# Performance work log

Hardware: AMD Instinct MI355X
Metric: run time of the kernel (lower is better)

## Reference

```python
import jax, jax.numpy as jnp
import numpy as np

BETA = 0.25


def setup_inputs() -> dict:
    key = jax.random.key(0)
    k1, k2 = jax.random.split(key)
    B, T, D, K = 64, 256, 512, 8192
    latents = jax.random.normal(k1, (B, T, D), dtype=jnp.float32)
    # nn.Embedding weight initialized uniform(-1/K, 1/K)
    emb = jax.random.uniform(k2, (K, D), dtype=jnp.float32, minval=-1.0 / K, maxval=1.0 / K)
    return {"latents": latents, "emb": emb}


def reference(latents, emb):
    B, T, D = latents.shape
    K = emb.shape[0]
    flat = latents.reshape(B * T, D)  # [N, D]
    # squared euclidean distances: [N, K]
    dist = (
        jnp.sum(flat ** 2, axis=1, keepdims=True)
        + jnp.sum(emb ** 2, axis=1)
        - 2.0 * flat @ emb.T
    )
    encoding_inds = jnp.argmin(dist, axis=1)  # [N]
    # one-hot @ emb == direct gather
    quantized = emb[encoding_inds].reshape(B, T, D)
    # losses (per-token mean over feature dim)
    q_sg = jax.lax.stop_gradient(quantized)
    l_sg = jax.lax.stop_gradient(latents)
    commitment_loss = jnp.mean((q_sg - latents) ** 2, axis=-1)  # [B, T]
    embedding_loss = jnp.mean((quantized - l_sg) ** 2, axis=-1)  # [B, T]
    vq_loss = embedding_loss + BETA * commitment_loss
    # straight-through estimator
    quantized_st = latents + jax.lax.stop_gradient(quantized - latents)
    return quantized_st, vq_loss, encoding_inds[None, :]  # inds as [1, N] like .t()
```

## Files before the change

### kernel.cpp

```cpp
#include <hip/hip_runtime.h>


#define D_DIM   512
#define K_CODES 8192
#define N_TOK   16384

typedef int i32x4  __attribute__((ext_vector_type(4)));
typedef int i32x16 __attribute__((ext_vector_type(16)));

__device__ __forceinline__ float np_pairwise_sq(const float* __restrict__ a) {
    float blk[4];
#pragma unroll
    for (int b = 0; b < 4; ++b) {
        const float* p = a + b * 128;
        float r[8];
#pragma unroll
        for (int j = 0; j < 8; ++j) { double d = (double)p[j]; r[j] = (float)(d * d); }
        for (int i = 8; i < 128; i += 8) {
#pragma unroll
            for (int j = 0; j < 8; ++j) { double d = (double)p[i + j]; r[j] = r[j] + (float)(d * d); }
        }
        blk[b] = ((r[0] + r[1]) + (r[2] + r[3])) + ((r[4] + r[5]) + (r[6] + r[7]));
    }
    return (blk[0] + blk[1]) + (blk[2] + blk[3]);
}

__device__ __forceinline__ unsigned q4pack(float4 v, float sc) {
    int q0 = (int)rintf(fminf(fmaxf(v.x * sc, -127.f), 127.f));
    int q1 = (int)rintf(fminf(fmaxf(v.y * sc, -127.f), 127.f));
    int q2 = (int)rintf(fminf(fmaxf(v.z * sc, -127.f), 127.f));
    int q3 = (int)rintf(fminf(fmaxf(v.w * sc, -127.f), 127.f));
    return (unsigned)(q0 & 255) | ((unsigned)(q1 & 255) << 8)
         | ((unsigned)(q2 & 255) << 16) | ((unsigned)(q3 & 255) << 24);
}

__global__ __launch_bounds__(256) void vq_prep(
    const float* __restrict__ X, const float* __restrict__ E,
    unsigned char* __restrict__ Xq, unsigned char* __restrict__ Eq,
    float* __restrict__ sx, float* __restrict__ se)
{
    const int bid = blockIdx.x;
    const int t = threadIdx.x;
    if (bid < 2048) {
        int tid = bid * 256 + t;
        int tb = tid >> 12, rem = tid & 4095;
        int line = rem >> 6, lane = rem & 63;
        int s = line >> 2, tf = line & 3;
        int token = tb * 128 + tf * 32 + (lane & 31);
        int d0 = s * 32 + (lane >> 5) * 16;
        const float4* p = (const float4*)(X + (size_t)token * D_DIM + d0);
        const float sc = 127.0f / 6.0f;
        uint4 o = make_uint4(q4pack(p[0], sc), q4pack(p[1], sc), q4pack(p[2], sc), q4pack(p[3], sc));
        *(uint4*)(Xq + (size_t)tb * 65536 + (size_t)line * 1024 + (size_t)lane * 16) = o;
    } else if (bid < 3072) {
        int tid = (bid - 2048) * 256 + t;
        int cb = tid >> 10, rem = tid & 1023;
        int s = rem >> 6, lane = rem & 63;
        int code = cb * 32 + (lane & 31);
        int d0 = s * 32 + (lane >> 5) * 16;
        const float4* p = (const float4*)(E + (size_t)code * D_DIM + d0);
        const float sc = 1040384.0f;
        uint4 o = make_uint4(q4pack(p[0], sc), q4pack(p[1], sc), q4pack(p[2], sc), q4pack(p[3], sc));
        *(uint4*)(Eq + (size_t)cb * 16384 + (size_t)s * 1024 + (size_t)lane * 16) = o;
    } else {
        int wv = (bid - 3072) * 4 + (t >> 6);
        int sub = (t >> 5) & 1, l32 = t & 31;
        int row = wv * 2 + sub;
        const float* p;
        float* dst;
        if (row < N_TOK) { p = X + (size_t)row * D_DIM; dst = sx + row; }
        else if (row < N_TOK + K_CODES) { p = E + (size_t)(row - N_TOK) * D_DIM; dst = se + (row - N_TOK); }
        else return;
        int b = l32 >> 3, rr = l32 & 7;
        const float* q = p + b * 128 + rr;
        double d0 = (double)q[0];
        float r = (float)(d0 * d0);
#pragma unroll
        for (int i = 1; i < 16; ++i) { double d = (double)q[8 * i]; r = r + (float)(d * d); }
#pragma unroll
        for (int m = 1; m <= 16; m <<= 1) r = r + __shfl_xor(r, m);
        if (l32 == 0) *dst = r;
    }
}

#define MFMA8(A, B, C) C = __builtin_amdgcn_mfma_i32_32x32x32_i8(A, B, C, 0, 0, 0)

#define UPD(T, P) { int _p = (P); \
    int _mn = _p < m0[T] ? _p : m0[T]; \
    m1[T] = _mn > m1[T] ? _mn : m1[T]; \
    m0[T] = _p > m0[T] ? _p : m0[T]; }

#define BLOAD(d0_, d1_, d2_, d3_, sidx) { int _o = ((sidx) & 15) * 4096 + laneB; \
    d0_ = *(const i32x4*)(smemB + _o); \
    d1_ = *(const i32x4*)(smemB + _o + 1024); \
    d2_ = *(const i32x4*)(smemB + _o + 2048); \
    d3_ = *(const i32x4*)(smemB + _o + 3072); }

#define STEP(Af, B0_, B1_, B2_, B3_) { \
    MFMA8(Af, B0_, a0); MFMA8(Af, B1_, a1); MFMA8(Af, B2_, a2); MFMA8(Af, B3_, a3); }

__global__ __launch_bounds__(512, 2) void vq_gemm(
    const unsigned char* __restrict__ Xq, const unsigned char* __restrict__ Eq,
    float* __restrict__ vbuf, int* __restrict__ ibuf)
{
    __shared__ unsigned int smemU[16384];
    const int tid = threadIdx.x;
    const int lane = tid & 63, w = tid >> 6;
    const int hi5 = lane >> 5, l31 = lane & 31;
    const int laneB = lane * 16;

    const int bid  = blockIdx.x;
    const int xcd  = bid & 7, slot = bid >> 3;
    const int q    = xcd >> 2;
    const int tb   = (xcd & 3) * 32 + slot;

    const unsigned char* Ap = Eq + (size_t)(q * 128 + w) * 16384;

    i32x4 QA0 = *(const i32x4*)(Ap + 0 * 1024 + laneB);
    i32x4 QA1 = *(const i32x4*)(Ap + 1 * 1024 + laneB);
    i32x4 QA2 = *(const i32x4*)(Ap + 2 * 1024 + laneB);
    i32x4 QA3 = *(const i32x4*)(Ap + 3 * 1024 + laneB);
    i32x4 QB0 = *(const i32x4*)(Ap + 4 * 1024 + laneB);
    i32x4 QB1 = *(const i32x4*)(Ap + 5 * 1024 + laneB);
    i32x4 QB2 = *(const i32x4*)(Ap + 6 * 1024 + laneB);
    i32x4 QB3 = *(const i32x4*)(Ap + 7 * 1024 + laneB);

    {
        const unsigned char* src = Xq + (size_t)tb * 65536;
#pragma unroll
        for (int c = 0; c < 8; ++c) {
            int off  = (c * 512 + tid) * 16;
            int doff = (c * 512 + w * 64) * 16;
            __builtin_amdgcn_global_load_lds((const unsigned int*)(src + off),
                                             (unsigned int*)((unsigned char*)smemU + doff), 16, 0, 0);
        }
    }
    __syncthreads();

    const unsigned char* smemB = (const unsigned char*)smemU;

    int m0[4], m1[4];
#pragma unroll
    for (int tf = 0; tf < 4; ++tf) { m0[tf] = (int)0x80000000; m1[tf] = (int)0x80000000; }

    i32x4 BA0, BA1, BA2, BA3, BB0, BB1, BB2, BB3;
    i32x4 BC0, BC1, BC2, BC3, BD0, BD1, BD2, BD3;
    BLOAD(BA0, BA1, BA2, BA3, 0);
    BLOAD(BB0, BB1, BB2, BB3, 1);

#pragma unroll 1
    for (int ck = 0; ck < 16; ++ck) {
        i32x16 a0 = {}, a1 = {}, a2 = {}, a3 = {};

#pragma unroll 1
        for (int mq = 0; mq < 2; ++mq) {
            const int s0 = 8 * mq;
            BLOAD(BC0, BC1, BC2, BC3, s0 + 2); STEP(QA0, BA0, BA1, BA2, BA3);
            BLOAD(BD0, BD1, BD2, BD3, s0 + 3); STEP(QA1, BB0, BB1, BB2, BB3);
            BLOAD(BA0, BA1, BA2, BA3, s0 + 4); STEP(QA2, BC0, BC1, BC2, BC3);
            BLOAD(BB0, BB1, BB2, BB3, s0 + 5); STEP(QA3, BD0, BD1, BD2, BD3);
            if (mq < 1) {
                QA0 = *(const i32x4*)(Ap + (size_t)(s0 + 8)  * 1024 + laneB);
                QA1 = *(const i32x4*)(Ap + (size_t)(s0 + 9)  * 1024 + laneB);
                QA2 = *(const i32x4*)(Ap + (size_t)(s0 + 10) * 1024 + laneB);
                QA3 = *(const i32x4*)(Ap + (size_t)(s0 + 11) * 1024 + laneB);
            }
            BLOAD(BC0, BC1, BC2, BC3, s0 + 6); STEP(QB0, BA0, BA1, BA2, BA3);
            BLOAD(BD0, BD1, BD2, BD3, s0 + 7); STEP(QB1, BB0, BB1, BB2, BB3);
            BLOAD(BA0, BA1, BA2, BA3, s0 + 8); STEP(QB2, BC0, BC1, BC2, BC3);
            BLOAD(BB0, BB1, BB2, BB3, s0 + 9); STEP(QB3, BD0, BD1, BD2, BD3);
            if (mq < 1) {
                QB0 = *(const i32x4*)(Ap + (size_t)(s0 + 12) * 1024 + laneB);
                QB1 = *(const i32x4*)(Ap + (size_t)(s0 + 13) * 1024 + laneB);
                QB2 = *(const i32x4*)(Ap + (size_t)(s0 + 14) * 1024 + laneB);
                QB3 = *(const i32x4*)(Ap + (size_t)(s0 + 15) * 1024 + laneB);
            }
        }

        const unsigned char* Apn = Ap + 131072;
        if (ck < 15) {
            QA0 = *(const i32x4*)(Apn + 0 * 1024 + laneB);
            QA1 = *(const i32x4*)(Apn + 1 * 1024 + laneB);
            QA2 = *(const i32x4*)(Apn + 2 * 1024 + laneB);
            QA3 = *(const i32x4*)(Apn + 3 * 1024 + laneB);
            QB0 = *(const i32x4*)(Apn + 4 * 1024 + laneB);
            QB1 = *(const i32x4*)(Apn + 5 * 1024 + laneB);
            QB2 = *(const i32x4*)(Apn + 6 * 1024 + laneB);
            QB3 = *(const i32x4*)(Apn + 7 * 1024 + laneB);
        }
        __builtin_amdgcn_sched_barrier(0);

        const int cb = q * 128 + ck * 8 + w;
        const int binv = 8191 - (cb * 32 + 4 * hi5);
#pragma unroll
        for (int g = 0; g < 16; ++g) {
            const int bp = binv - ((g & 3) + 8 * (g >> 2));
            UPD(0, ((a0[g] >> 5) << 13) + bp);
            UPD(1, ((a1[g] >> 5) << 13) + bp);
            UPD(2, ((a2[g] >> 5) << 13) + bp);
            UPD(3, ((a3[g] >> 5) << 13) + bp);
        }
        Ap = Apn;
    }

#pragma unroll
    for (int tf = 0; tf < 4; ++tf) {
        int token = tb * 128 + tf * 32 + l31;
        int slot2 = q * 32 + w * 4 + hi5 * 2;
        size_t base = (size_t)token * 64 + slot2;
        vbuf[base]     = (float)(m0[tf] >> 13);
        ibuf[base]     = 8191 - (m0[tf] & 8191);
        vbuf[base + 1] = (float)(m1[tf] >> 13);
        ibuf[base + 1] = 8191 - (m1[tf] & 8191);
    }
}

__global__ __launch_bounds__(256) void vq_refine(
    const float* __restrict__ X, const float* __restrict__ E,
    const float* __restrict__ vbuf, const int* __restrict__ ibuf,
    const float* __restrict__ sx, const float* __restrict__ se,
    float* __restrict__ out_idx, float* __restrict__ outq, float* __restrict__ outl)
{
    int t = threadIdx.x;
    int n = blockIdx.x * 4 + (t >> 6);
    int lane = t & 63;

    float v = vbuf[(size_t)n * 64 + lane];
    int   ci = ibuf[(size_t)n * 64 + lane];
    float b0 = v;
#pragma unroll
    for (int m = 1; m <= 32; m <<= 1) b0 = fmaxf(b0, __shfl_xor(b0, m));

    unsigned long long mask = __ballot(v >= b0 - 200.0f);

    const float* xr = X + (size_t)n * D_DIM;
    float4 xa = ((const float4*)xr)[lane * 2];
    float4 xb = ((const float4*)xr)[lane * 2 + 1];
    float sxn = sx[n];

    float bd = 1e30f; int bi = 2147483647;
    while (mask) {
        int b = (int)__builtin_ctzll(mask);
        mask &= mask - 1;
        int idx = __shfl(ci, b);
        const float* er = E + (size_t)idx * D_DIM;
        float4 ea = ((const float4*)er)[lane * 2];
        float4 eb = ((const float4*)er)[lane * 2 + 1];
        double p = (double)xa.x * ea.x + (double)xa.y * ea.y + (double)xa.z * ea.z + (double)xa.w * ea.w
                 + (double)xb.x * eb.x + (double)xb.y * eb.y + (double)xb.z * eb.z + (double)xb.w * eb.w;
#pragma unroll
        for (int m = 1; m <= 32; m <<= 1) p = p + __shfl_xor(p, m);
        float M = (float)p;
        float S = sxn + se[idx];
        float d = S - 2.0f * M;
        if (d < bd || (d == bd && idx < bi)) { bd = d; bi = idx; }
    }
    if (lane == 0) out_idx[n] = (float)bi;

    const float* er = E + (size_t)bi * D_DIM;
    float4 ea = ((const float4*)er)[lane * 2];
    float4 eb = ((const float4*)er)[lane * 2 + 1];
    float4 da, db;
    da.x = ea.x - xa.x; da.y = ea.y - xa.y; da.z = ea.z - xa.z; da.w = ea.w - xa.w;
    db.x = eb.x - xb.x; db.y = eb.y - xb.y; db.z = eb.z - xb.z; db.w = eb.w - xb.w;
    float4 qa, qb;
    qa.x = xa.x + da.x; qa.y = xa.y + da.y; qa.z = xa.z + da.z; qa.w = xa.w + da.w;
    qb.x = xb.x + db.x; qb.y = xb.y + db.y; qb.z = xb.z + db.z; qb.w = xb.w + db.w;
    float4* qr = (float4*)(outq + (size_t)n * D_DIM);
    qr[lane * 2] = qa;
    qr[lane * 2 + 1] = qb;
    float s = da.x * da.x + da.y * da.y + da.z * da.z + da.w * da.w
            + db.x * db.x + db.y * db.y + db.z * db.z + db.w * db.w;
#pragma unroll
    for (int m = 1; m <= 32; m <<= 1) s += __shfl_xor(s, m);
    if (lane == 0) {
        float mmean = s * (1.0f / (float)D_DIM);
        outl[n] = mmean + 0.25f * mmean;
    }
}

__global__ __launch_bounds__(512) void vq_argmin_fb(
    const float* __restrict__ X, const float* __restrict__ E, float* __restrict__ out_idx)
{
    __shared__ __align__(16) unsigned char smem[48 * 1024];
    float4* Xs = (float4*)smem;
    float4* Es = (float4*)(smem + 16 * 1024);
    float*  cv = (float*)smem;
    int*    ci = (int*)(smem + 16 * 1024);
    const int t = threadIdx.x, tc = t & 31, tr = t >> 5;
    const int tok0 = blockIdx.x * 64;
    const float4* Xg = (const float4*)X;
    const float4* Eg = (const float4*)E;
    float v0[4], v1[4]; int i0[4], i1[4];
#pragma unroll
    for (int i = 0; i < 4; ++i) { v0[i] = -1e30f; v1[i] = -1e30f; i0[i] = 0; i1[i] = 1; }
    for (int kt = 0; kt < K_CODES / 128; ++kt) {
        float acc[4][4];
#pragma unroll
        for (int i = 0; i < 4; ++i)
#pragma unroll
            for (int j = 0; j < 4; ++j) acc[i][j] = 0.f;
        for (int dc = 0; dc < 8; ++dc) {
            __syncthreads();
#pragma unroll
            for (int s = 0; s < 2; ++s) {
                int id = t + s * 512; int rr = id >> 4, m = id & 15;
                Xs[rr * 16 + ((m + (rr >> 2)) & 15)] = Xg[(size_t)(tok0 + rr) * 128 + dc * 16 + m];
            }
#pragma unroll
            for (int s = 0; s < 4; ++s) {
                int id = t + s * 512; int rr = id >> 4, m = id & 15;
                Es[rr * 16 + ((m + (rr >> 2)) & 15)] = Eg[(size_t)(kt * 128 + rr) * 128 + dc * 16 + m];
            }
            __syncthreads();
#pragma unroll
            for (int dd4 = 0; dd4 < 16; ++dd4) {
                float4 xv[4], ev[4];
#pragma unroll
                for (int i = 0; i < 4; ++i) xv[i] = Xs[(4 * tr + i) * 16 + ((dd4 + tr) & 15)];
#pragma unroll
                for (int j = 0; j < 4; ++j) ev[j] = Es[(4 * tc + j) * 16 + ((dd4 + tc) & 15)];
#pragma unroll
                for (int i = 0; i < 4; ++i)
#pragma unroll
                    for (int j = 0; j < 4; ++j)
                        acc[i][j] += xv[i].x * ev[j].x + xv[i].y * ev[j].y + xv[i].z * ev[j].z + xv[i].w * ev[j].w;
            }
        }
#pragma unroll
        for (int i = 0; i < 4; ++i)
#pragma unroll
            for (int j = 0; j < 4; ++j) {
                float v = acc[i][j]; int idx = kt * 128 + 4 * tc + j;
                if (v > v0[i])      { v1[i] = v0[i]; i1[i] = i0[i]; v0[i] = v; i0[i] = idx; }
                else if (v > v1[i]) { v1[i] = v; i1[i] = idx; }
            }
    }
    __syncthreads();
#pragma unroll
    for (int i = 0; i < 4; ++i) {
        int row = 4 * tr + i;
        cv[row * 64 + 2 * tc] = v0[i];     ci[row * 64 + 2 * tc] = i0[i];
        cv[row * 64 + 2 * tc + 1] = v1[i]; ci[row * 64 + 2 * tc + 1] = i1[i];
    }
    __syncthreads();
    if (t < 64) {
        const int row = t;
        float b0 = -1e30f;
        for (int s = 0; s < 64; ++s) b0 = fmaxf(b0, cv[row * 64 + s]);
        const float* xr = X + (size_t)(tok0 + row) * D_DIM;
        const float sumx2 = np_pairwise_sq(xr);
        float bd = 1e30f; int bi = 0x7fffffff;
        for (int s = 0; s < 64; ++s) {
            float v = cv[row * 64 + s];
            if (v < b0 - 1.0e-4f) continue;
            int idx = ci[row * 64 + s];
            const float* er = E + (size_t)idx * D_DIM;
            double acc = 0.0;
            for (int d0 = 0; d0 < D_DIM; ++d0) acc += (double)xr[d0] * (double)er[d0];
            float M = (float)acc;
            float se2 = np_pairwise_sq(er);
            float S = sumx2 + se2;
            float d = S - 2.0f * M;
            if (d < bd || (d == bd && idx < bi)) { bd = d; bi = idx; }
        }
        out_idx[tok0 + row] = (float)bi;
    }
}

__global__ __launch_bounds__(256) void vq_gather_fb(
    const float* __restrict__ X, const float* __restrict__ E,
    const float* __restrict__ idxf, float* __restrict__ outq, float* __restrict__ outl)
{
    const int t = threadIdx.x;
    const int h = t >> 7, tt = t & 127;
    const int n = blockIdx.x * 2 + h;
    const int idx = (int)idxf[n];
    const float4* xr = (const float4*)(X + (size_t)n * D_DIM);
    const float4* er = (const float4*)(E + (size_t)idx * D_DIM);
    float4* qr = (float4*)(outq + (size_t)n * D_DIM);
    float4 x = xr[tt], e = er[tt];
    float4 dl; dl.x = e.x - x.x; dl.y = e.y - x.y; dl.z = e.z - x.z; dl.w = e.w - x.w;
    float4 qv; qv.x = x.x + dl.x; qv.y = x.y + dl.y; qv.z = x.z + dl.z; qv.w = x.w + dl.w;
    qr[tt] = qv;
    float s = dl.x * dl.x + dl.y * dl.y + dl.z * dl.z + dl.w * dl.w;
#pragma unroll
    for (int off = 32; off > 0; off >>= 1) s += __shfl_down(s, off, 64);
    __shared__ float red[4];
    if ((t & 63) == 0) red[t >> 6] = s;
    __syncthreads();
    if (tt == 0) {
        float m = (red[h * 2] + red[h * 2 + 1]) * (1.0f / (float)D_DIM);
        outl[n] = m + 0.25f * m;
    }
}

extern "C" void kernel_launch(void* const* d_in, const int* in_sizes, int n_in,
                              void* d_out, int out_size, void* d_ws, size_t ws_size,
                              hipStream_t stream) {
    const float* X = (const float*)d_in[0];
    const float* E = (const float*)d_in[1];
    float* out  = (float*)d_out;
    float* outq = out;
    float* outl = out + (size_t)N_TOK * D_DIM;
    float* outi = outl + N_TOK;

    const size_t WS_NEED = 21069824;
    if (ws_size >= WS_NEED) {
        unsigned char* ws = (unsigned char*)d_ws;
        unsigned char* Xq = ws;
        unsigned char* Eq = ws + 8388608;
        float* vbuf = (float*)(ws + 12582912);
        int*   ibuf = (int*)(ws + 16777216);
        float* sx   = (float*)(ws + 20971520);
        float* se   = (float*)(ws + 21037056);
        vq_prep<<<6144, 256, 0, stream>>>(X, E, Xq, Eq, sx, se);
        vq_gemm<<<256, 512, 0, stream>>>(Xq, Eq, vbuf, ibuf);
        vq_refine<<<4096, 256, 0, stream>>>(X, E, vbuf, ibuf, sx, se, outi, outq, outl);
    } else {
        vq_argmin_fb<<<N_TOK / 64, 512, 0, stream>>>(X, E, outi);
        vq_gather_fb<<<8192, 256, 0, stream>>>(X, E, outi, outq, outl);
    }
}
```

Before: 122.4 us.

## Double-buffer MFMA accumulators to overlap argmin selection with next chunk GEMM

Restructures the main GEMM loop so two sets of i32x16 accumulators alternate: while one code chunk's MFMAs run, the top-2 selection of the previous chunk's results executes, removing the serialized sched_barrier plus select tail of each iteration. The inner mq loop is fully unrolled and the loop manually unrolled by two with prologue/epilogue. This doubles accumulator register usage (64 extra VGPRs/AGPRs), which risks spills or reduced occupancy under launch_bounds(512,2).

Result: slower. 385.1 us (+214.6%).

```diff
diff --git a/kernel.cpp b/kernel.cpp
--- a/kernel.cpp
+++ b/kernel.cpp
@@ -90,14 +90,63 @@
     m1[T] = _mn > m1[T] ? _mn : m1[T]; \
     m0[T] = _p > m0[T] ? _p : m0[T]; }
 
-#define BLOAD(d0_, d1_, d2_, d3_, sidx) { int _o = ((sidx) & 15) * 4096 + laneB; \
-    d0_ = *(const i32x4*)(smemB + _o); \
-    d1_ = *(const i32x4*)(smemB + _o + 1024); \
-    d2_ = *(const i32x4*)(smemB + _o + 2048); \
-    d3_ = *(const i32x4*)(smemB + _o + 3072); }
-
-#define STEP(Af, B0_, B1_, B2_, B3_) { \
-    MFMA8(Af, B0_, a0); MFMA8(Af, B1_, a1); MFMA8(Af, B2_, a2); MFMA8(Af, B3_, a3); }
+#define BLOADS(BS, sidx) { \
+    BS##0 = *(const i32x4*)(smemB + ((sidx) & 15) * 4096 + laneB); \
+    BS##1 = *(const i32x4*)(smemB + ((sidx) & 15) * 4096 + 1024 + laneB); \
+    BS##2 = *(const i32x4*)(smemB + ((sidx) & 15) * 4096 + 2048 + laneB); \
+    BS##3 = *(const i32x4*)(smemB + ((sidx) & 15) * 4096 + 3072 + laneB); }
+
+#define STEPX(Af, BS, c0, c1, c2, c3) { \
+    MFMA8(Af, BS##0, c0); MFMA8(Af, BS##1, c1); \
+    MFMA8(Af, BS##2, c2); MFMA8(Af, BS##3, c3); }
+
+#define CKBODY(c0, c1, c2, c3) { \
+    BLOADS(BC, 2);  STEPX(QA0, BA, c0, c1, c2, c3); \
+    BLOADS(BD, 3);  STEPX(QA1, BB, c0, c1, c2, c3); \
+    BLOADS(BA, 4);  STEPX(QA2, BC, c0, c1, c2, c3); \
+    BLOADS(BB, 5);  STEPX(QA3, BD, c0, c1, c2, c3); \
+    QA0 = *(const i32x4*)(Ap + 8  * 1024 + laneB); \
+    QA1 = *(const i32x4*)(Ap + 9  * 1024 + laneB); \
+    QA2 = *(const i32x4*)(Ap + 10 * 1024 + laneB); \
+    QA3 = *(const i32x4*)(Ap + 11 * 1024 + laneB); \
+    BLOADS(BC, 6);  STEPX(QB0, BA, c0, c1, c2, c3); \
+    BLOADS(BD, 7);  STEPX(QB1, BB, c0, c1, c2, c3); \
+    BLOADS(BA, 8);  STEPX(QB2, BC, c0, c1, c2, c3); \
+    BLOADS(BB, 9);  STEPX(QB3, BD, c0, c1, c2, c3); \
+    QB0 = *(const i32x4*)(Ap + 12 * 1024 + laneB); \
+    QB1 = *(const i32x4*)(Ap + 13 * 1024 + laneB); \
+    QB2 = *(const i32x4*)(Ap + 14 * 1024 + laneB); \
+    QB3 = *(const i32x4*)(Ap + 15 * 1024 + laneB); \
+    BLOADS(BC, 10); STEPX(QA0, BA, c0, c1, c2, c3); \
+    BLOADS(BD, 11); STEPX(QA1, BB, c0, c1, c2, c3); \
+    BLOADS(BA, 12); STEPX(QA2, BC, c0, c1, c2, c3); \
+    BLOADS(BB, 13); STEPX(QA3, BD, c0, c1, c2, c3); \
+    BLOADS(BC, 14); STEPX(QB0, BA, c0, c1, c2, c3); \
+    BLOADS(BD, 15); STEPX(QB1, BB, c0, c1, c2, c3); \
+    BLOADS(BA, 0);  STEPX(QB2, BC, c0, c1, c2, c3); \
+    BLOADS(BB, 1);  STEPX(QB3, BD, c0, c1, c2, c3); }
+
+#define APROLOGUE() { \
+    QA0 = *(const i32x4*)(Ap + 131072 + 0 * 1024 + laneB); \
+    QA1 = *(const i32x4*)(Ap + 131072 + 1 * 1024 + laneB); \
+    QA2 = *(const i32x4*)(Ap + 131072 + 2 * 1024 + laneB); \
+    QA3 = *(const i32x4*)(Ap + 131072 + 3 * 1024 + laneB); \
+    QB0 = *(const i32x4*)(Ap + 131072 + 4 * 1024 + laneB); \
+    QB1 = *(const i32x4*)(Ap + 131072 + 5 * 1024 + laneB); \
+    QB2 = *(const i32x4*)(Ap + 131072 + 6 * 1024 + laneB); \
+    QB3 = *(const i32x4*)(Ap + 131072 + 7 * 1024 + laneB); \
+    Ap += 131072; }
+
+#define SELECT(c0, c1, c2, c3) { \
+    _Pragma("unroll") \
+    for (int g = 0; g < 16; ++g) { \
+        const int bp = binv - ((g & 3) + 8 * (g >> 2)); \
+        UPD(0, ((c0[g] >> 5) << 13) + bp); \
+        UPD(1, ((c1[g] >> 5) << 13) + bp); \
+        UPD(2, ((c2[g] >> 5) << 13) + bp); \
+        UPD(3, ((c3[g] >> 5) << 13) + bp); \
+    } \
+    binv -= 256; }
 
 __global__ __launch_bounds__(512, 2) void vq_gemm(
     const unsigned char* __restrict__ Xq, const unsigned char* __restrict__ Eq,
@@ -145,63 +194,33 @@
 
     i32x4 BA0, BA1, BA2, BA3, BB0, BB1, BB2, BB3;
     i32x4 BC0, BC1, BC2, BC3, BD0, BD1, BD2, BD3;
-    BLOAD(BA0, BA1, BA2, BA3, 0);
-    BLOAD(BB0, BB1, BB2, BB3, 1);
+    BLOADS(BA, 0);
+    BLOADS(BB, 1);
+
+    int binv = 8191 - (q * 4096 + w * 32 + 4 * hi5);
+
+    const i32x16 Z = {};
+    i32x16 xa0 = Z, xa1 = Z, xa2 = Z, xa3 = Z;
+    i32x16 xb0, xb1, xb2, xb3;
+
+    CKBODY(xa0, xa1, xa2, xa3);
+    APROLOGUE();
 
 #pragma unroll 1
-    for (int ck = 0; ck < 16; ++ck) {
-        i32x16 a0 = {}, a1 = {}, a2 = {}, a3 = {};
-
-#pragma unroll 1
-        for (int mq = 0; mq < 2; ++mq) {
-            const int s0 = 8 * mq;
-            BLOAD(BC0, BC1, BC2, BC3, s0 + 2); STEP(QA0, BA0, BA1, BA2, BA3);
-            BLOAD(BD0, BD1, BD2, BD3, s0 + 3); STEP(QA1, BB0, BB1, BB2, BB3);
-            BLOAD(BA0, BA1, BA2, BA3, s0 + 4); STEP(QA2, BC0, BC1, BC2, BC3);
-            BLOAD(BB0, BB1, BB2, BB3, s0 + 5); STEP(QA3, BD0, BD1, BD2, BD3);
-            if (mq < 1) {
-                QA0 = *(const i32x4*)(Ap + (size_t)(s0 + 8)  * 1024 + laneB);
-                QA1 = *(const i32x4*)(Ap + (size_t)(s0 + 9)  * 1024 + laneB);
-                QA2 = *(const i32x4*)(Ap + (size_t)(s0 + 10) * 1024 + laneB);
-                QA3 = *(const i32x4*)(Ap + (size_t)(s0 + 11) * 1024 + laneB);
-            }
-            BLOAD(BC0, BC1, BC2, BC3, s0 + 6); STEP(QB0, BA0, BA1, BA2, BA3);
-            BLOAD(BD0, BD1, BD2, BD3, s0 + 7); STEP(QB1, BB0, BB1, BB2, BB3);
-            BLOAD(BA0, BA1, BA2, BA3, s0 + 8); STEP(QB2, BC0, BC1, BC2, BC3);
-            BLOAD(BB0, BB1, BB2, BB3, s0 + 9); STEP(QB3, BD0, BD1, BD2, BD3);
-            if (mq < 1) {
-                QB0 = *(const i32x4*)(Ap + (size_t)(s0 + 12) * 1024 + laneB);
-                QB1 = *(const i32x4*)(Ap + (size_t)(s0 + 13) * 1024 + laneB);
-                QB2 = *(const i32x4*)(Ap + (size_t)(s0 + 14) * 1024 + laneB);
-                QB3 = *(const i32x4*)(Ap + (size_t)(s0 + 15) * 1024 + laneB);
-            }
-        }
-
-        const unsigned char* Apn = Ap + 131072;
-        if (ck < 15) {
-            QA0 = *(const i32x4*)(Apn + 0 * 1024 + laneB);
-            QA1 = *(const i32x4*)(Apn + 1 * 1024 + laneB);
-            QA2 = *(const i32x4*)(Apn + 2 * 1024 + laneB);
-            QA3 = *(const i32x4*)(Apn + 3 * 1024 + laneB);
-            QB0 = *(const i32x4*)(Apn + 4 * 1024 + laneB);
-            QB1 = *(const i32x4*)(Apn + 5 * 1024 + laneB);
-            QB2 = *(const i32x4*)(Apn + 6 * 1024 + laneB);
-            QB3 = *(const i32x4*)(Apn + 7 * 1024 + laneB);
-        }
-        __builtin_amdgcn_sched_barrier(0);
-
-        const int cb = q * 128 + ck * 8 + w;
-        const int binv = 8191 - (cb * 32 + 4 * hi5);
-#pragma unroll
-        for (int g = 0; g < 16; ++g) {
-            const int bp = binv - ((g & 3) + 8 * (g >> 2));
-            UPD(0, ((a0[g] >> 5) << 13) + bp);
-            UPD(1, ((a1[g] >> 5) << 13) + bp);
-            UPD(2, ((a2[g] >> 5) << 13) + bp);
-            UPD(3, ((a3[g] >> 5) << 13) + bp);
-        }
-        Ap = Apn;
-    }
+    for (int it = 0; it < 7; ++it) {
+        xb0 = Z; xb1 = Z; xb2 = Z; xb3 = Z;
+        CKBODY(xb0, xb1, xb2, xb3);
+        APROLOGUE();
+        SELECT(xa0, xa1, xa2, xa3);
+        xa0 = Z; xa1 = Z; xa2 = Z; xa3 = Z;
+        CKBODY(xa0, xa1, xa2, xa3);
+        APROLOGUE();
+        SELECT(xb0, xb1, xb2, xb3);
+    }
+    xb0 = Z; xb1 = Z; xb2 = Z; xb3 = Z;
+    CKBODY(xb0, xb1, xb2, xb3);
+    SELECT(xa0, xa1, xa2, xa3);
+    SELECT(xb0, xb1, xb2, xb3);
 
 #pragma unroll
     for (int tf = 0; tf < 4; ++tf) {
```
